# Optimization experiments

Measured on AMD Instinct MI355X. Metric: run time of the kernel, lower is better.

## Reference

```python
import jax, jax.numpy as jnp
import numpy as np

EMBED_DIM = 1024
NUM_HEADS = 16
HEAD_DIM = EMBED_DIM // NUM_HEADS
GLOBAL_HEADS = 1
LOCAL_K = 128
SCALE = HEAD_DIM ** -0.5


def setup_inputs() -> dict:
    key = jax.random.key(0)
    ks = jax.random.split(key, 9)
    B, n = 4, 2048
    s = 1.0 / np.sqrt(EMBED_DIM)  # torch Linear default uniform(-1/sqrt(in), 1/sqrt(in))
    def lin(k):
        kw, kb = jax.random.split(k)
        W = jax.random.uniform(kw, (EMBED_DIM, EMBED_DIM), jnp.float32, -s, s)
        b = jax.random.uniform(kb, (EMBED_DIM,), jnp.float32, -s, s)
        return W, b
    wq, bq = lin(ks[0])
    wk, bk = lin(ks[1])
    wv, bv = lin(ks[2])
    wo, bo = lin(ks[3])
    x = jax.random.normal(ks[4], (B, n, EMBED_DIM), jnp.float32)
    return {"x": x, "wq": wq, "bq": bq, "wk": wk, "bk": bk,
            "wv": wv, "bv": bv, "wo": wo, "bo": bo}


def _attend(x, wq, bq, wk, bk, wv, bv, wo, bo):
    B, n, E = x.shape
    H, D = NUM_HEADS, HEAD_DIM
    def proj(W, b):
        t = x @ W.T + b                       # [B, n, E]
        return t.reshape(B, n, H, D).transpose(0, 2, 1, 3)  # [B, H, n, D]
    q, k, v = proj(wq, bq), proj(wk, bk), proj(wv, bv)
    scores = jnp.einsum('bhqd,bhkd->bhqk', q, k) * SCALE  # [B, H, n, n]
    idx = jnp.arange(n)
    band = jnp.abs(idx[:, None] - idx[None, :]) <= LOCAL_K  # [n, n] True = allowed
    is_global = jnp.arange(H) < GLOBAL_HEADS
    mask = band[None, :, :] | is_global[:, None, None]      # [H, n, n]
    scores = jnp.where(mask[None], scores, -jnp.inf)
    attn = jax.nn.softmax(scores, axis=-1)   # dropout is identity (p=0 / eval)
    out = jnp.einsum('bhqk,bhkd->bhqd', attn, v)
    out = out.transpose(0, 2, 1, 3).reshape(B, n, E)
    return out @ wo.T + bo


def reference(x, wq, bq, wk, bk, wv, bv, wo, bo):
    return _attend(x, wq, bq, wk, bk, wv, bv, wo, bo)
```

## Files before the change

### kernel.cpp

```cpp
#include <hip/hip_runtime.h>

typedef __attribute__((ext_vector_type(4))) float f32x4;
typedef __attribute__((ext_vector_type(8))) short s16x8;

#define GLDS(gsrc, ldst) \
  __builtin_amdgcn_global_load_lds((const __attribute__((address_space(1))) void*)(gsrc), \
                                   (__attribute__((address_space(3))) void*)(ldst), 16, 0, 0)

__device__ __forceinline__ ushort f2bf(float f) {
  union { float f; unsigned u; } x; x.f = f;
  unsigned r = (x.u + 0x7FFFu + ((x.u >> 16) & 1u)) >> 16;
  return (ushort)r;
}

__global__ __launch_bounds__(256) void castk(const float* __restrict__ in,
                                             ushort* __restrict__ outp, int n) {
  int i = (blockIdx.x * 256 + threadIdx.x) * 4;
  if (i >= n) return;
  float4 v = *(const float4*)(in + i);
  ushort4 r;
  r.x = f2bf(v.x); r.y = f2bf(v.y); r.z = f2bf(v.z); r.w = f2bf(v.w);
  *(ushort4*)(outp + i) = r;
}

__global__ __launch_bounds__(256) void castw(const float* __restrict__ w0, const float* __restrict__ w1,
                                             const float* __restrict__ w2, const float* __restrict__ w3,
                                             ushort* __restrict__ o0, ushort* __restrict__ o1,
                                             ushort* __restrict__ o2, ushort* __restrict__ o3) {
  int bid = blockIdx.x;
  int sel = bid >> 10;
  const float* in = (sel == 0) ? w0 : (sel == 1) ? w1 : (sel == 2) ? w2 : w3;
  ushort* outp    = (sel == 0) ? o0 : (sel == 1) ? o1 : (sel == 2) ? o2 : o3;
  int i = ((bid & 1023) * 256 + threadIdx.x) * 4;
  float4 v = *(const float4*)(in + i);
  ushort4 r;
  r.x = f2bf(v.x); r.y = f2bf(v.y); r.z = f2bf(v.z); r.w = f2bf(v.w);
  *(ushort4*)(outp + i) = r;
}

#define BM 128
#define BN 128
#define BK 32

__global__ __launch_bounds__(256) void gemm_bt(
    const ushort* __restrict__ A, const ushort* __restrict__ Bt,
    const float* __restrict__ bias0, const float* __restrict__ bias1,
    const float* __restrict__ bias2,
    void* __restrict__ Cout, int M, int N, int K, int outBf16)
{
  __shared__ __align__(16) ushort As[BM * BK];
  __shared__ __align__(16) ushort Bs[BN * BK];
  const int tid = threadIdx.x;
  const int w = tid >> 6, lane = tid & 63;
  const int wr = w >> 1, wc = w & 1;
  const int lrow = lane & 15, lg = lane >> 4;
  const int mblk = blockIdx.y * BM, nblk = blockIdx.x * BN;
  const int c0 = 2 * w, c1 = 2 * w + 1;
  const int ar0 = 16 * c0 + (lane >> 2), ar1 = 16 * c1 + (lane >> 2);
  const int akk = 8 * (lane & 3);
  const ushort* Ab = A + (size_t)mblk * K + akk;
  const ushort* Bb = Bt + (size_t)nblk * K + akk;
  const f32x4 zero = {0.f, 0.f, 0.f, 0.f};
  f32x4 acc[4][4];
#pragma unroll
  for (int m = 0; m < 4; m++)
#pragma unroll
    for (int n = 0; n < 4; n++) acc[m][n] = zero;

  for (int kt = 0; kt < K; kt += BK) {
    GLDS(Ab + (size_t)ar0 * K + kt, &As[512 * c0]);
    GLDS(Ab + (size_t)ar1 * K + kt, &As[512 * c1]);
    GLDS(Bb + (size_t)ar0 * K + kt, &Bs[512 * c0]);
    GLDS(Bb + (size_t)ar1 * K + kt, &Bs[512 * c1]);
    __syncthreads();
    s16x8 af[4], bfr[4];
#pragma unroll
    for (int m = 0; m < 4; m++)
      af[m] = *(const s16x8*)&As[(64 * wr + 16 * m + lrow) * BK + 8 * lg];
#pragma unroll
    for (int n = 0; n < 4; n++)
      bfr[n] = *(const s16x8*)&Bs[(64 * wc + 16 * n + lrow) * BK + 8 * lg];
#pragma unroll
    for (int m = 0; m < 4; m++)
#pragma unroll
      for (int n = 0; n < 4; n++)
        acc[m][n] = __builtin_amdgcn_mfma_f32_16x16x32_bf16(af[m], bfr[n], acc[m][n], 0, 0, 0);
    __syncthreads();
  }

#pragma unroll
  for (int m = 0; m < 4; m++) {
    const int row = mblk + 64 * wr + 16 * m + 4 * lg;
#pragma unroll
    for (int n = 0; n < 4; n++) {
      const int col = nblk + 64 * wc + 16 * n + lrow;
      float bias;
      if (bias1) bias = (col < 1024) ? bias0[col]
                       : (col < 2048 ? bias1[col - 1024] : bias2[col - 2048]);
      else bias = bias0[col];
      f32x4 v = acc[m][n];
      if (outBf16) {
        ushort* C = (ushort*)Cout;
#pragma unroll
        for (int i = 0; i < 4; i++) C[(size_t)(row + i) * N + col] = f2bf(v[i] + bias);
      } else {
        float* C = (float*)Cout;
#pragma unroll
        for (int i = 0; i < 4; i++) C[(size_t)(row + i) * N + col] = v[i] + bias;
      }
    }
  }
}

__global__ __launch_bounds__(256) void attn_kernel(const ushort* __restrict__ qkv,
                                                   ushort* __restrict__ outp,
                                                   float* __restrict__ oPart,
                                                   float* __restrict__ mPart,
                                                   float* __restrict__ lPart)
{
  __shared__ __align__(16) ushort Ks[64 * 64];
  __shared__ __align__(16) ushort Vt[64 * 64];
  __shared__ __align__(16) ushort Ps[4][16 * 40];

  const int tid = threadIdx.x;
  const int w = tid >> 6, lane = tid & 63;
  const int lrow = lane & 15, lg = lane >> 4;

  const int bid = (blockIdx.x & 7) * 368 + (blockIdx.x >> 3);
  int h, b, bx, kv_lo, kv_hi, chunk = 0;
  bool isGlobal;
  if (bid < 1024) {
    isGlobal = true; h = 0;
    chunk = bid >> 7;
    int qb = bid & 127;
    b = qb >> 5; bx = qb & 31;
    kv_lo = chunk * 256; kv_hi = kv_lo + 256;
  } else {
    isGlobal = false;
    int t = bid - 1024;
    h = 1 + (t >> 7);
    int qb = t & 127;
    b = qb >> 5; bx = qb & 31;
    kv_lo = bx * 64 - 128; if (kv_lo < 0) kv_lo = 0;
    kv_hi = bx * 64 + 192; if (kv_hi > 2048) kv_hi = 2048;
  }
  const int q0b = bx * 64;
  const int q0 = q0b + w * 16;
  const ushort* Qp = qkv + (size_t)b * 2048 * 3072 + h * 64;
  const ushort* Kp = Qp + 1024;
  const ushort* Vp = Qp + 2048;

  s16x8 qf0 = *(const s16x8*)(Qp + (size_t)(q0 + lrow) * 3072 + 8 * lg);
  s16x8 qf1 = *(const s16x8*)(Qp + (size_t)(q0 + lrow) * 3072 + 32 + 8 * lg);

  const f32x4 zero = {0.f, 0.f, 0.f, 0.f};
  f32x4 o[4];
  o[0] = zero; o[1] = zero; o[2] = zero; o[3] = zero;
  float mrun = -3e38f, lsum = 0.f;
  const int q_abs = q0 + lrow;
  const float SCL = 0.18033688011112042f;

  const int sp = tid >> 3;
  const int sg = tid & 7;
  const int kr0 = tid >> 3;
  const int kc = tid & 7;
  const int vx = (lrow & 7) ^ (lrow >> 3);

  for (int kv = kv_lo; kv < kv_hi; kv += 64) {
    const bool needMask = !isGlobal && (kv < q0b - 64 || kv + 64 > q0b + 128);

    const ushort* vrow = Vp + (size_t)(kv + 2 * sp) * 3072 + 8 * sg;
    s16x8 vlo = *(const s16x8*)vrow;
    s16x8 vhi = *(const s16x8*)(vrow + 3072);

    __syncthreads();

    GLDS(Kp + (size_t)(kv + kr0) * 3072 + 8 * (kc ^ (kr0 & 7)), &Ks[w * 512]);
    GLDS(Kp + (size_t)(kv + 32 + kr0) * 3072 + 8 * (kc ^ (kr0 & 7)), &Ks[2048 + w * 512]);

#pragma unroll
    for (int j = 0; j < 8; j++) {
      const int d = 8 * sg + j;
      const int r = 2 * sp;
      uint pk = (uint)(ushort)vlo[j] | ((uint)(ushort)vhi[j] << 16);
      *(uint*)&Vt[d * 64 + ((((r >> 3) ^ j ^ sg) & 7) << 3) + (r & 7)] = pk;
    }
    __syncthreads();

#pragma unroll
    for (int s = 0; s < 2; s++) {
      const int kb = kv + 32 * s;
      const int rs = 32 * s;
      s16x8 kA0 = *(const s16x8*)&Ks[(rs + lrow) * 64      + ((( lg      ^ (lrow & 7)) & 7) << 3)];
      s16x8 kA1 = *(const s16x8*)&Ks[(rs + lrow) * 64      + ((((4 + lg) ^ (lrow & 7)) & 7) << 3)];
      s16x8 kB0 = *(const s16x8*)&Ks[(rs + 16 + lrow) * 64 + ((( lg      ^ (lrow & 7)) & 7) << 3)];
      s16x8 kB1 = *(const s16x8*)&Ks[(rs + 16 + lrow) * 64 + ((((4 + lg) ^ (lrow & 7)) & 7) << 3)];

      f32x4 sA = __builtin_amdgcn_mfma_f32_16x16x32_bf16(kA0, qf0, zero, 0, 0, 0);
      sA = __builtin_amdgcn_mfma_f32_16x16x32_bf16(kA1, qf1, sA, 0, 0, 0);
      f32x4 sB = __builtin_amdgcn_mfma_f32_16x16x32_bf16(kB0, qf0, zero, 0, 0, 0);
      sB = __builtin_amdgcn_mfma_f32_16x16x32_bf16(kB1, qf1, sB, 0, 0, 0);

      float pA[4], pB[4];
      float rowmax = -3e38f;
      if (needMask) {
#pragma unroll
        for (int i = 0; i < 4; i++) {
          int kaA = kb + 4 * lg + i;
          int dq = q_abs - kaA;
          float va = (dq <= 128 && dq >= -128) ? sA[i] * SCL : -1e30f;
          pA[i] = va; rowmax = fmaxf(rowmax, va);
          int dqb = dq - 16;
          float vb = (dqb <= 128 && dqb >= -128) ? sB[i] * SCL : -1e30f;
          pB[i] = vb; rowmax = fmaxf(rowmax, vb);
        }
      } else {
#pragma unroll
        for (int i = 0; i < 4; i++) {
          pA[i] = sA[i] * SCL; pB[i] = sB[i] * SCL;
          rowmax = fmaxf(rowmax, fmaxf(pA[i], pB[i]));
        }
      }
      rowmax = fmaxf(rowmax, __shfl_xor(rowmax, 16));
      rowmax = fmaxf(rowmax, __shfl_xor(rowmax, 32));

      if (!__all(rowmax <= mrun + 8.f)) {
        float mnew = fmaxf(mrun, rowmax);
        float alpha = exp2f(mrun - mnew);
        mrun = mnew;
        lsum *= alpha;
        float a0 = __shfl(alpha, 4 * lg + 0);
        float a1 = __shfl(alpha, 4 * lg + 1);
        float a2 = __shfl(alpha, 4 * lg + 2);
        float a3 = __shfl(alpha, 4 * lg + 3);
#pragma unroll
        for (int c = 0; c < 4; c++) {
          o[c][0] *= a0; o[c][1] *= a1; o[c][2] *= a2; o[c][3] *= a3;
        }
      }

      float rsum = 0.f;
      if (needMask) {
#pragma unroll
        for (int i = 0; i < 4; i++) {
          pA[i] = (pA[i] > -1e29f) ? exp2f(pA[i] - mrun) : 0.f;
          pB[i] = (pB[i] > -1e29f) ? exp2f(pB[i] - mrun) : 0.f;
          rsum += pA[i] + pB[i];
        }
      } else {
#pragma unroll
        for (int i = 0; i < 4; i++) {
          pA[i] = exp2f(pA[i] - mrun);
          pB[i] = exp2f(pB[i] - mrun);
          rsum += pA[i] + pB[i];
        }
      }
      rsum += __shfl_xor(rsum, 16);
      rsum += __shfl_xor(rsum, 32);
      lsum += rsum;

      {
        ushort* P = &Ps[w][lrow * 40];
        *(uint*)&P[4 * lg]      = (uint)f2bf(pA[0]) | ((uint)f2bf(pA[1]) << 16);
        *(uint*)&P[4 * lg + 2]  = (uint)f2bf(pA[2]) | ((uint)f2bf(pA[3]) << 16);
        *(uint*)&P[16 + 4 * lg] = (uint)f2bf(pB[0]) | ((uint)f2bf(pB[1]) << 16);
        *(uint*)&P[18 + 4 * lg] = (uint)f2bf(pB[2]) | ((uint)f2bf(pB[3]) << 16);
      }
      s16x8 paf = *(const s16x8*)&Ps[w][lrow * 40 + 8 * lg];

#pragma unroll
      for (int c = 0; c < 4; c++) {
        const int d = 16 * c + lrow;
        s16x8 vf = *(const s16x8*)&Vt[d * 64 + ((((4 * s + lg) ^ vx ^ (2 * c)) & 7) << 3)];
        o[c] = __builtin_amdgcn_mfma_f32_16x16x32_bf16(paf, vf, o[c], 0, 0, 0);
      }
    }
  }

  if (isGlobal) {
    const size_t rbase = (size_t)(chunk * 4 + b) * 2048 + q0;
    if (lg == 0) {
      mPart[rbase + lrow] = mrun;
      lPart[rbase + lrow] = lsum;
    }
#pragma unroll
    for (int c = 0; c < 4; c++)
#pragma unroll
      for (int i = 0; i < 4; i++)
        oPart[(rbase + 4 * lg + i) * 64 + 16 * c + lrow] = o[c][i];
  } else {
    float li0 = 1.f / __shfl(lsum, 4 * lg + 0);
    float li1 = 1.f / __shfl(lsum, 4 * lg + 1);
    float li2 = 1.f / __shfl(lsum, 4 * lg + 2);
    float li3 = 1.f / __shfl(lsum, 4 * lg + 3);
    size_t orow = (size_t)(b * 2048 + q0 + 4 * lg);
#pragma unroll
    for (int c = 0; c < 4; c++) {
      outp[(orow + 0) * 1024 + h * 64 + 16 * c + lrow] = f2bf(o[c][0] * li0);
      outp[(orow + 1) * 1024 + h * 64 + 16 * c + lrow] = f2bf(o[c][1] * li1);
      outp[(orow + 2) * 1024 + h * 64 + 16 * c + lrow] = f2bf(o[c][2] * li2);
      outp[(orow + 3) * 1024 + h * 64 + 16 * c + lrow] = f2bf(o[c][3] * li3);
    }
  }
}

__global__ __launch_bounds__(256) void combine_kernel(const float* __restrict__ oPart,
                                                      const float* __restrict__ mPart,
                                                      const float* __restrict__ lPart,
                                                      ushort* __restrict__ attno) {
  const int tid = threadIdx.x;
  const int row = blockIdx.x * 64 + (tid >> 2);
  const int d0 = (tid & 3) * 16;
  float m[8], l[8], M = -3e38f;
#pragma unroll
  for (int p = 0; p < 8; p++) {
    m[p] = mPart[p * 8192 + row];
    l[p] = lPart[p * 8192 + row];
    M = fmaxf(M, m[p]);
  }
  float L = 0.f, wgt[8];
#pragma unroll
  for (int p = 0; p < 8; p++) { wgt[p] = exp2f(m[p] - M); L += wgt[p] * l[p]; }
  float inv = 1.f / L;
  float acc[16];
#pragma unroll
  for (int j = 0; j < 16; j++) acc[j] = 0.f;
#pragma unroll
  for (int p = 0; p < 8; p++) {
    const float* op = oPart + ((size_t)p * 8192 + row) * 64 + d0;
    float wv = wgt[p];
#pragma unroll
    for (int j = 0; j < 16; j += 4) {
      float4 v = *(const float4*)(op + j);
      acc[j]     += wv * v.x; acc[j + 1] += wv * v.y;
      acc[j + 2] += wv * v.z; acc[j + 3] += wv * v.w;
    }
  }
  ushort* dst = attno + (size_t)row * 1024 + d0;
#pragma unroll
  for (int j = 0; j < 16; j++) dst[j] = f2bf(acc[j] * inv);
}

extern "C" void kernel_launch(void* const* d_in, const int* in_sizes, int n_in,
                              void* d_out, int out_size, void* d_ws, size_t ws_size,
                              hipStream_t stream) {
  const float* x  = (const float*)d_in[0];
  const float* wq = (const float*)d_in[1];
  const float* bq = (const float*)d_in[2];
  const float* wk = (const float*)d_in[3];
  const float* bk = (const float*)d_in[4];
  const float* wv = (const float*)d_in[5];
  const float* bv = (const float*)d_in[6];
  const float* wo = (const float*)d_in[7];
  const float* bo = (const float*)d_in[8];

  char* ws = (char*)d_ws;
  ushort* xb    = (ushort*)(ws);
  ushort* wqkvb = (ushort*)(ws + 16777216);
  ushort* wob   = (ushort*)(ws + 23068672);
  ushort* qkvb  = (ushort*)(ws + 25165824);
  ushort* attno = (ushort*)(ws + 75497472);
  float* oPart = (float*)(ws);
  float* mPart = (float*)(ws + 16777216);
  float* lPart = (float*)(ws + 16777216 + 262144);

  castk<<<8192, 256, 0, stream>>>(x, xb, 8388608);
  castw<<<4096, 256, 0, stream>>>(wq, wk, wv, wo,
                                  wqkvb, wqkvb + 1048576, wqkvb + 2097152, wob);

  gemm_bt<<<dim3(24, 64), 256, 0, stream>>>(xb, wqkvb, bq, bk, bv,
                                            (void*)qkvb, 8192, 3072, 1024, 1);

  attn_kernel<<<2944, 256, 0, stream>>>(qkvb, attno, oPart, mPart, lPart);
  combine_kernel<<<128, 256, 0, stream>>>(oPart, mPart, lPart, attno);

  gemm_bt<<<dim3(8, 64), 256, 0, stream>>>(attno, wob, bo, nullptr, nullptr,
                                           (void*)d_out, 8192, 1024, 1024, 0);
}
```

Baseline: 183.4 us.

## Replace GEMM with 128x256 triple-buffered swizzled-LDS kernel and coalesced epilogue

Replaces the simple 128x128 single-buffer GEMM with a 512-thread 128x256-tile kernel. It uses BK=64, a three-stage global_load_lds pipeline with explicit vmcnt waits, and an XOR-swizzled LDS layout to avoid bank conflicts. It also adds a remapping of workgroup IDs across XCDs and s_setprio around the MFMA bursts. The epilogue now stages results through LDS so global stores are wide and coalesced instead of scattered scalar writes. The cost is higher LDS use (144KB), which limits occupancy, plus more complex wait-count logic.

```diff
diff --git a/kernel.cpp b/kernel.cpp
--- a/kernel.cpp
+++ b/kernel.cpp
@@ -38,28 +38,50 @@
   *(ushort4*)(outp + i) = r;
 }
 
-#define BM 128
-#define BN 128
-#define BK 32
-
-__global__ __launch_bounds__(256) void gemm_bt(
+template<int OUTBF16>
+__global__ __launch_bounds__(512, 2) void gemm256(
     const ushort* __restrict__ A, const ushort* __restrict__ Bt,
     const float* __restrict__ bias0, const float* __restrict__ bias1,
     const float* __restrict__ bias2,
-    void* __restrict__ Cout, int M, int N, int K, int outBf16)
+    void* __restrict__ Cout, int M, int N, int K, int nxn)
 {
-  __shared__ __align__(16) ushort As[BM * BK];
-  __shared__ __align__(16) ushort Bs[BN * BK];
+  __shared__ __align__(16) ushort lds[73728];
   const int tid = threadIdx.x;
   const int w = tid >> 6, lane = tid & 63;
-  const int wr = w >> 1, wc = w & 1;
   const int lrow = lane & 15, lg = lane >> 4;
-  const int mblk = blockIdx.y * BM, nblk = blockIdx.x * BN;
-  const int c0 = 2 * w, c1 = 2 * w + 1;
-  const int ar0 = 16 * c0 + (lane >> 2), ar1 = 16 * c1 + (lane >> 2);
-  const int akk = 8 * (lane & 3);
-  const ushort* Ab = A + (size_t)mblk * K + akk;
-  const ushort* Bb = Bt + (size_t)nblk * K + akk;
+  const int wm = w >> 2, wn = w & 3;
+  const int cpx = gridDim.x >> 3;
+  const int wgid = ((int)blockIdx.x & 7) * cpx + ((int)blockIdx.x >> 3);
+  const int mblk = (wgid / nxn) * 128;
+  const int nblk = (wgid % nxn) * 256;
+  const int NT = K >> 6;
+
+  const int srow = tid >> 3;
+  const int scol = 8 * ((tid & 7) ^ (srow & 7));
+  const ushort* Abase = A + (size_t)(mblk + srow) * K + scol;
+  const ushort* Bbase = Bt + (size_t)(nblk + srow) * K + scol;
+  const size_t rstep = (size_t)64 * K;
+  const int dA = w * 512;
+  const int dB = 8192 + w * 512;
+
+#define STAGE_A(kt, bf) { \
+    GLDS(Abase + (size_t)(kt) * 64,         &lds[(bf) * 24576 + dA]); \
+    GLDS(Abase + (size_t)(kt) * 64 + rstep, &lds[(bf) * 24576 + dA + 4096]); }
+#define STAGE_B(kt, bf) { \
+    GLDS(Bbase + (size_t)(kt) * 64,             &lds[(bf) * 24576 + dB]); \
+    GLDS(Bbase + (size_t)(kt) * 64 + rstep,     &lds[(bf) * 24576 + dB + 4096]); \
+    GLDS(Bbase + (size_t)(kt) * 64 + 2 * rstep, &lds[(bf) * 24576 + dB + 8192]); \
+    GLDS(Bbase + (size_t)(kt) * 64 + 3 * rstep, &lds[(bf) * 24576 + dB + 12288]); }
+
+  int offA[4][2], offB[4][2];
+#pragma unroll
+  for (int m = 0; m < 4; m++)
+#pragma unroll
+    for (int kk = 0; kk < 2; kk++) {
+      offA[m][kk] = (wm * 64 + m * 16 + lrow) * 64 + (((kk * 4 + lg) ^ (lrow & 7)) << 3);
+      offB[m][kk] = 8192 + (wn * 64 + m * 16 + lrow) * 64 + (((kk * 4 + lg) ^ (lrow & 7)) << 3);
+    }
+
   const f32x4 zero = {0.f, 0.f, 0.f, 0.f};
   f32x4 acc[4][4];
 #pragma unroll
@@ -67,47 +89,99 @@
 #pragma unroll
     for (int n = 0; n < 4; n++) acc[m][n] = zero;
 
-  for (int kt = 0; kt < K; kt += BK) {
-    GLDS(Ab + (size_t)ar0 * K + kt, &As[512 * c0]);
-    GLDS(Ab + (size_t)ar1 * K + kt, &As[512 * c1]);
-    GLDS(Bb + (size_t)ar0 * K + kt, &Bs[512 * c0]);
-    GLDS(Bb + (size_t)ar1 * K + kt, &Bs[512 * c1]);
+  STAGE_A(0, 0); STAGE_B(0, 0);
+  if (NT > 1) { STAGE_A(1, 1); STAGE_B(1, 1); }
+
+  int b = 0;
+  for (int t = 0; t < NT; ++t) {
+    if (t < NT - 1) { asm volatile("s_waitcnt vmcnt(6)" ::: "memory"); }
+    else            { asm volatile("s_waitcnt vmcnt(0)" ::: "memory"); }
+    __builtin_amdgcn_s_barrier();
+    const int bb = b * 24576;
+    const int t2 = t + 2;
+    const int b2 = (b >= 1) ? b - 1 : 2;
+
+    if (t2 < NT) STAGE_A(t2, b2);
+    {
+      s16x8 af[4], bf_[4];
+#pragma unroll
+      for (int m = 0; m < 4; m++) af[m] = *(const s16x8*)&lds[bb + offA[m][0]];
+#pragma unroll
+      for (int n = 0; n < 4; n++) bf_[n] = *(const s16x8*)&lds[bb + offB[n][0]];
+      __builtin_amdgcn_s_setprio(1);
+#pragma unroll
+      for (int m = 0; m < 4; m++)
+#pragma unroll
+        for (int n = 0; n < 4; n++)
+          acc[m][n] = __builtin_amdgcn_mfma_f32_16x16x32_bf16(af[m], bf_[n], acc[m][n], 0, 0, 0);
+      __builtin_amdgcn_s_setprio(0);
+    }
+    if (t2 < NT) STAGE_B(t2, b2);
+    {
+      s16x8 af[4], bf_[4];
+#pragma unroll
+      for (int m = 0; m < 4; m++) af[m] = *(const s16x8*)&lds[bb + offA[m][1]];
+#pragma unroll
+      for (int n = 0; n < 4; n++) bf_[n] = *(const s16x8*)&lds[bb + offB[n][1]];
+      __builtin_amdgcn_s_setprio(1);
+#pragma unroll
+      for (int m = 0; m < 4; m++)
+#pragma unroll
+        for (int n = 0; n < 4; n++)
+          acc[m][n] = __builtin_amdgcn_mfma_f32_16x16x32_bf16(af[m], bf_[n], acc[m][n], 0, 0, 0);
+      __builtin_amdgcn_s_setprio(0);
+    }
+    b = (b == 2) ? 0 : b + 1;
+  }
+#undef STAGE_A
+#undef STAGE_B
+
+  float bias_n[4];
+#pragma unroll
+  for (int n = 0; n < 4; n++) {
+    const int col = nblk + wn * 64 + n * 16 + lrow;
+    if (bias1) bias_n[n] = (col < 1024) ? bias0[col]
+                          : (col < 2048 ? bias1[col - 1024] : bias2[col - 2048]);
+    else bias_n[n] = bias0[col];
+  }
+
+  __syncthreads();
+
+  if (OUTBF16) {
+    ushort* Ct = lds;
+#pragma unroll
+    for (int m = 0; m < 4; m++)
+#pragma unroll
+      for (int n = 0; n < 4; n++)
+#pragma unroll
+        for (int i = 0; i < 4; i++)
+          Ct[(wm * 64 + m * 16 + 4 * lg + i) * 256 + wn * 64 + n * 16 + lrow] =
+              f2bf(acc[m][n][i] + bias_n[n]);
     __syncthreads();
-    s16x8 af[4], bfr[4];
+    ushort* Cg = (ushort*)Cout;
+#pragma unroll
+    for (int r = 0; r < 8; r++) {
+      const int row = r * 16 + (tid >> 5);
+      const int col = (tid & 31) * 8;
+      *(s16x8*)&Cg[(size_t)(mblk + row) * N + nblk + col] = *(const s16x8*)&lds[r * 4096 + tid * 8];
+    }
+  } else {
+    float* Cf = (float*)lds;
 #pragma unroll
     for (int m = 0; m < 4; m++)
-      af[m] = *(const s16x8*)&As[(64 * wr + 16 * m + lrow) * BK + 8 * lg];
-#pragma unroll
-    for (int n = 0; n < 4; n++)
-      bfr[n] = *(const s16x8*)&Bs[(64 * wc + 16 * n + lrow) * BK + 8 * lg];
-#pragma unroll
-    for (int m = 0; m < 4; m++)
 #pragma unroll
       for (int n = 0; n < 4; n++)
-        acc[m][n] = __builtin_amdgcn_mfma_f32_16x16x32_bf16(af[m], bfr[n], acc[m][n], 0, 0, 0);
+#pragma unroll
+        for (int i = 0; i < 4; i++)
+          Cf[(wm * 64 + m * 16 + 4 * lg + i) * 256 + wn * 64 + n * 16 + lrow] =
+              acc[m][n][i] + bias_n[n];
     __syncthreads();
-  }
-
-#pragma unroll
-  for (int m = 0; m < 4; m++) {
-    const int row = mblk + 64 * wr + 16 * m + 4 * lg;
-#pragma unroll
-    for (int n = 0; n < 4; n++) {
-      const int col = nblk + 64 * wc + 16 * n + lrow;
-      float bias;
-      if (bias1) bias = (col < 1024) ? bias0[col]
-                       : (col < 2048 ? bias1[col - 1024] : bias2[col - 2048]);
-      else bias = bias0[col];
-      f32x4 v = acc[m][n];
-      if (outBf16) {
-        ushort* C = (ushort*)Cout;
-#pragma unroll
-        for (int i = 0; i < 4; i++) C[(size_t)(row + i) * N + col] = f2bf(v[i] + bias);
-      } else {
-        float* C = (float*)Cout;
-#pragma unroll
-        for (int i = 0; i < 4; i++) C[(size_t)(row + i) * N + col] = v[i] + bias;
-      }
+    float* Cg = (float*)Cout;
+#pragma unroll
+    for (int r = 0; r < 16; r++) {
+      const int row = r * 8 + (tid >> 6);
+      const int col = (tid & 63) * 4;
+      *(float4*)&Cg[(size_t)(mblk + row) * N + nblk + col] = *(const float4*)&Cf[r * 2048 + tid * 4];
     }
   }
 }
@@ -368,12 +442,12 @@
   castw<<<4096, 256, 0, stream>>>(wq, wk, wv, wo,
                                   wqkvb, wqkvb + 1048576, wqkvb + 2097152, wob);
 
-  gemm_bt<<<dim3(24, 64), 256, 0, stream>>>(xb, wqkvb, bq, bk, bv,
-                                            (void*)qkvb, 8192, 3072, 1024, 1);
+  gemm256<1><<<768, 512, 0, stream>>>(xb, wqkvb, bq, bk, bv,
+                                      (void*)qkvb, 8192, 3072, 1024, 12);
 
   attn_kernel<<<2944, 256, 0, stream>>>(qkvb, attno, oPart, mPart, lPart);
   combine_kernel<<<128, 256, 0, stream>>>(oPart, mPart, lPart, attno);
 
-  gemm_bt<<<dim3(8, 64), 256, 0, stream>>>(attno, wob, bo, nullptr, nullptr,
-                                           (void*)d_out, 8192, 1024, 1024, 0);
-}
+  gemm256<0><<<256, 512, 0, stream>>>(attno, wob, bo, nullptr, nullptr,
+                                      (void*)d_out, 8192, 1024, 1024, 4);
+}
```

Result: faster. 167.1 us (-8.9%).

## Replace GEMM with 256x256 tile, double-buffered, swizzled LDS pipelined kernel

Applied to the files above, without the earlier changes.

Replaces the simple 128x128x32 single-buffer bf16 GEMM with a 512-thread 256x256 tile kernel using BK=64, double-buffered LDS fed by global_load_lds, XOR-swizzled LDS layout, and a quadrant-interleaved schedule that overlaps loads with MFMA. It adds explicit vmcnt waits, setprio around MFMA bursts, XCD-aware block remapping, and an LDS-staged epilogue that writes output in coalesced vectors. The goal is to remove stalls from the synchronous load/compute loop and uncoalesced stores. The larger tiles yield fewer workgroups (384 and 128), which may underfill the GPU, especially for the output projection.

```diff
diff --git a/kernel.cpp b/kernel.cpp
--- a/kernel.cpp
+++ b/kernel.cpp
@@ -11,6 +11,12 @@
   union { float f; unsigned u; } x; x.f = f;
   unsigned r = (x.u + 0x7FFFu + ((x.u >> 16) & 1u)) >> 16;
   return (ushort)r;
+}
+
+template<int N> __device__ __forceinline__ void waitvm() {
+  if constexpr (N == 0) asm volatile("s_waitcnt vmcnt(0)" ::: "memory");
+  else if constexpr (N == 4) asm volatile("s_waitcnt vmcnt(4)" ::: "memory");
+  else if constexpr (N == 8) asm volatile("s_waitcnt vmcnt(8)" ::: "memory");
 }
 
 __global__ __launch_bounds__(256) void castk(const float* __restrict__ in,
@@ -38,75 +44,184 @@
   *(ushort4*)(outp + i) = r;
 }
 
-#define BM 128
-#define BN 128
-#define BK 32
-
-__global__ __launch_bounds__(256) void gemm_bt(
+template<int OUTBF16>
+__global__ __launch_bounds__(512) void gemmQ(
     const ushort* __restrict__ A, const ushort* __restrict__ Bt,
     const float* __restrict__ bias0, const float* __restrict__ bias1,
     const float* __restrict__ bias2,
-    void* __restrict__ Cout, int M, int N, int K, int outBf16)
+    void* __restrict__ Cout, int M, int N, int K, int nxn)
 {
-  __shared__ __align__(16) ushort As[BM * BK];
-  __shared__ __align__(16) ushort Bs[BN * BK];
+  constexpr int SB = 32768;
+  __shared__ __align__(16) ushort lds[65536];
+
   const int tid = threadIdx.x;
   const int w = tid >> 6, lane = tid & 63;
-  const int wr = w >> 1, wc = w & 1;
   const int lrow = lane & 15, lg = lane >> 4;
-  const int mblk = blockIdx.y * BM, nblk = blockIdx.x * BN;
-  const int c0 = 2 * w, c1 = 2 * w + 1;
-  const int ar0 = 16 * c0 + (lane >> 2), ar1 = 16 * c1 + (lane >> 2);
-  const int akk = 8 * (lane & 3);
-  const ushort* Ab = A + (size_t)mblk * K + akk;
-  const ushort* Bb = Bt + (size_t)nblk * K + akk;
+  const int wm2a = (w >> 2) * 64, wn2a = (w & 3) * 32;
+  const int cpx = gridDim.x >> 3;
+  const int wgid = ((int)blockIdx.x & 7) * cpx + ((int)blockIdx.x >> 3);
+  const int mblk = (wgid / nxn) * 256;
+  const int nblk = (wgid % nxn) * 256;
+  const int NT = K >> 6, NI = NT >> 1;
+
+  const int sg8 = 8 * ((tid & 7) ^ ((tid >> 3) & 7));
+  const ushort* As0 = A + (size_t)(mblk + (tid >> 3)) * K + sg8;
+  const ushort* Bs0 = Bt + (size_t)(nblk + (tid >> 3)) * K + sg8;
+  const size_t r64 = (size_t)64 * K;
+  const int wl512 = w * 512;
+
+  auto stage = [&](int isB, int kt, int half, int bufb) {
+    const ushort* s = (isB ? Bs0 : As0) + (size_t)kt * 64 + (size_t)(half * 128) * K;
+    const int d = bufb + isB * 16384 + half * 8192 + wl512;
+    GLDS(s, &lds[d]);
+    GLDS(s + r64, &lds[d + 4096]);
+  };
+
+  const int axk0 = ((lg) ^ (lrow & 7)) << 3;
+  const int axk1 = ((4 + lg) ^ (lrow & 7)) << 3;
+  const int arow = (wm2a + lrow) * 64;
+  const int brow = 16384 + (wn2a + lrow) * 64;
+
+  s16x8 af[4][2], bf0[2][2], bf1[2][2];
   const f32x4 zero = {0.f, 0.f, 0.f, 0.f};
-  f32x4 acc[4][4];
-#pragma unroll
-  for (int m = 0; m < 4; m++)
-#pragma unroll
-    for (int n = 0; n < 4; n++) acc[m][n] = zero;
-
-  for (int kt = 0; kt < K; kt += BK) {
-    GLDS(Ab + (size_t)ar0 * K + kt, &As[512 * c0]);
-    GLDS(Ab + (size_t)ar1 * K + kt, &As[512 * c1]);
-    GLDS(Bb + (size_t)ar0 * K + kt, &Bs[512 * c0]);
-    GLDS(Bb + (size_t)ar1 * K + kt, &Bs[512 * c1]);
+  f32x4 acc[2][2][4][2];
+#pragma unroll
+  for (int qm = 0; qm < 2; qm++)
+#pragma unroll
+    for (int qn = 0; qn < 2; qn++)
+#pragma unroll
+      for (int mf = 0; mf < 4; mf++)
+#pragma unroll
+        for (int nf = 0; nf < 2; nf++) acc[qm][qn][mf][nf] = zero;
+
+#define LOADA(qm, bb) { \
+  _Pragma("unroll") for (int mf = 0; mf < 4; mf++) { \
+    af[mf][0] = *(const s16x8*)&lds[(bb) + (qm) * 8192 + arow + mf * 1024 + axk0]; \
+    af[mf][1] = *(const s16x8*)&lds[(bb) + (qm) * 8192 + arow + mf * 1024 + axk1]; } }
+#define LOADB(qn, bb, bfr) { \
+  _Pragma("unroll") for (int nf = 0; nf < 2; nf++) { \
+    bfr[nf][0] = *(const s16x8*)&lds[(bb) + (qn) * 8192 + brow + nf * 1024 + axk0]; \
+    bfr[nf][1] = *(const s16x8*)&lds[(bb) + (qn) * 8192 + brow + nf * 1024 + axk1]; } }
+#define MMA(qm, qn, bfr) { \
+  __builtin_amdgcn_s_setprio(1); \
+  _Pragma("unroll") for (int mf = 0; mf < 4; mf++) \
+    _Pragma("unroll") for (int nf = 0; nf < 2; nf++) { \
+      acc[qm][qn][mf][nf] = __builtin_amdgcn_mfma_f32_16x16x32_bf16(af[mf][0], bfr[nf][0], acc[qm][qn][mf][nf], 0, 0, 0); \
+      acc[qm][qn][mf][nf] = __builtin_amdgcn_mfma_f32_16x16x32_bf16(af[mf][1], bfr[nf][1], acc[qm][qn][mf][nf], 0, 0, 0); } \
+  __builtin_amdgcn_s_setprio(0); }
+#define BAR() __builtin_amdgcn_s_barrier()
+
+  stage(0, 0, 0, 0);  stage(0, 0, 1, 0);  stage(1, 0, 0, 0);  stage(1, 0, 1, 0);
+  stage(0, 1, 0, SB); stage(0, 1, 1, SB); stage(1, 1, 0, SB); stage(1, 1, 1, SB);
+  waitvm<8>(); BAR();
+
+  for (int it = 0; it < NI; ++it) {
+    const bool sB1 = (it > 0);
+    const bool sA2 = (2 * it + 2 < NT);
+    const bool sB2 = (2 * it + 3 < NT);
+    const int kb1 = 2 * it + 1, ka2 = 2 * it + 2, kb2 = 2 * it + 3;
+
+    LOADA(0, 0); LOADB(0, 0, bf0);
+    if (sB1) stage(0, kb1, 1, SB);
+    BAR(); MMA(0, 0, bf0); BAR();
+    LOADB(1, 0, bf1);
+    if (sB1) stage(1, kb1, 0, SB);
+    BAR(); MMA(0, 1, bf1); BAR();
+    LOADA(1, 0);
+    if (sA2) stage(0, ka2, 0, 0);
+    BAR(); MMA(1, 1, bf1);
+    BAR();
+    if (sA2) stage(1, ka2, 1, 0);
+    BAR(); MMA(1, 0, bf0);
+    if (it == NI - 1) waitvm<0>(); else waitvm<4>();
+    BAR();
+
+    LOADA(0, SB); LOADB(0, SB, bf0);
+    if (sA2) stage(0, ka2, 1, 0);
+    BAR(); MMA(0, 0, bf0); BAR();
+    LOADB(1, SB, bf1);
+    if (sA2) stage(1, ka2, 0, 0);
+    BAR(); MMA(0, 1, bf1); BAR();
+    LOADA(1, SB);
+    if (sB2) stage(0, kb2, 0, SB);
+    BAR(); MMA(1, 1, bf1); BAR();
+    if (sB2) stage(1, kb2, 1, SB);
+    BAR(); MMA(1, 0, bf0);
+    if (it + 1 < NI) {
+      if (it + 1 == NI - 1) waitvm<0>(); else waitvm<4>();
+      BAR();
+    }
+  }
+#undef LOADA
+#undef LOADB
+#undef MMA
+#undef BAR
+
+  float bias_n[2][2];
+#pragma unroll
+  for (int qn = 0; qn < 2; qn++)
+#pragma unroll
+    for (int nf = 0; nf < 2; nf++) {
+      const int col = nblk + qn * 128 + wn2a + nf * 16 + lrow;
+      if (bias1) bias_n[qn][nf] = (col < 1024) ? bias0[col]
+                                 : (col < 2048 ? bias1[col - 1024] : bias2[col - 2048]);
+      else bias_n[qn][nf] = bias0[col];
+    }
+
+  __syncthreads();
+
+  if constexpr (OUTBF16) {
+    ushort* Ct = lds;
+#pragma unroll
+    for (int qm = 0; qm < 2; qm++)
+#pragma unroll
+      for (int qn = 0; qn < 2; qn++)
+#pragma unroll
+        for (int mf = 0; mf < 4; mf++)
+#pragma unroll
+          for (int nf = 0; nf < 2; nf++) {
+            f32x4 v = acc[qm][qn][mf][nf];
+#pragma unroll
+            for (int i = 0; i < 4; i++)
+              Ct[(qm * 128 + wm2a + mf * 16 + 4 * lg + i) * 256 +
+                 qn * 128 + wn2a + nf * 16 + lrow] = f2bf(v[i] + bias_n[qn][nf]);
+          }
     __syncthreads();
-    s16x8 af[4], bfr[4];
-#pragma unroll
-    for (int m = 0; m < 4; m++)
-      af[m] = *(const s16x8*)&As[(64 * wr + 16 * m + lrow) * BK + 8 * lg];
-#pragma unroll
-    for (int n = 0; n < 4; n++)
-      bfr[n] = *(const s16x8*)&Bs[(64 * wc + 16 * n + lrow) * BK + 8 * lg];
-#pragma unroll
-    for (int m = 0; m < 4; m++)
-#pragma unroll
-      for (int n = 0; n < 4; n++)
-        acc[m][n] = __builtin_amdgcn_mfma_f32_16x16x32_bf16(af[m], bfr[n], acc[m][n], 0, 0, 0);
-    __syncthreads();
-  }
-
-#pragma unroll
-  for (int m = 0; m < 4; m++) {
-    const int row = mblk + 64 * wr + 16 * m + 4 * lg;
-#pragma unroll
-    for (int n = 0; n < 4; n++) {
-      const int col = nblk + 64 * wc + 16 * n + lrow;
-      float bias;
-      if (bias1) bias = (col < 1024) ? bias0[col]
-                       : (col < 2048 ? bias1[col - 1024] : bias2[col - 2048]);
-      else bias = bias0[col];
-      f32x4 v = acc[m][n];
-      if (outBf16) {
-        ushort* C = (ushort*)Cout;
-#pragma unroll
-        for (int i = 0; i < 4; i++) C[(size_t)(row + i) * N + col] = f2bf(v[i] + bias);
-      } else {
-        float* C = (float*)Cout;
-#pragma unroll
-        for (int i = 0; i < 4; i++) C[(size_t)(row + i) * N + col] = v[i] + bias;
+    ushort* Cg = (ushort*)Cout;
+#pragma unroll
+    for (int p = 0; p < 16; p++) {
+      const unsigned g = p * 512 + tid;
+      const unsigned row = g >> 5, c8 = g & 31;
+      *(s16x8*)&Cg[(size_t)(mblk + row) * N + nblk + c8 * 8] = *(const s16x8*)&lds[g * 8];
+    }
+  } else {
+    float* Cf = (float*)lds;
+    float* Cg = (float*)Cout;
+#pragma unroll
+    for (int c = 0; c < 4; c++) {
+      __syncthreads();
+      if ((w >> 2) == (c & 1)) {
+        const int qm = c >> 1;
+#pragma unroll
+        for (int qn = 0; qn < 2; qn++)
+#pragma unroll
+          for (int mf = 0; mf < 4; mf++)
+#pragma unroll
+            for (int nf = 0; nf < 2; nf++) {
+              f32x4 v = acc[qm][qn][mf][nf];
+#pragma unroll
+              for (int i = 0; i < 4; i++)
+                Cf[(mf * 16 + 4 * lg + i) * 256 + qn * 128 + wn2a + nf * 16 + lrow] =
+                    v[i] + bias_n[qn][nf];
+            }
+      }
+      __syncthreads();
+#pragma unroll
+      for (int p = 0; p < 8; p++) {
+        const unsigned fg = p * 512 + tid;
+        const unsigned row = fg >> 6, c4 = fg & 63;
+        *(float4*)&Cg[(size_t)(mblk + c * 64 + row) * N + nblk + c4 * 4] =
+            *(const float4*)&Cf[fg * 4];
       }
     }
   }
@@ -368,12 +483,12 @@
   castw<<<4096, 256, 0, stream>>>(wq, wk, wv, wo,
                                   wqkvb, wqkvb + 1048576, wqkvb + 2097152, wob);
 
-  gemm_bt<<<dim3(24, 64), 256, 0, stream>>>(xb, wqkvb, bq, bk, bv,
-                                            (void*)qkvb, 8192, 3072, 1024, 1);
+  gemmQ<1><<<384, 512, 0, stream>>>(xb, wqkvb, bq, bk, bv,
+                                    (void*)qkvb, 8192, 3072, 1024, 12);
 
   attn_kernel<<<2944, 256, 0, stream>>>(qkvb, attno, oPart, mPart, lPart);
   combine_kernel<<<128, 256, 0, stream>>>(oPart, mPart, lPart, attno);
 
-  gemm_bt<<<dim3(8, 64), 256, 0, stream>>>(attno, wob, bo, nullptr, nullptr,
-                                           (void*)d_out, 8192, 1024, 1024, 0);
-}
+  gemmQ<0><<<128, 512, 0, stream>>>(attno, wob, bo, nullptr, nullptr,
+                                    (void*)d_out, 8192, 1024, 1024, 4);
+}
```

New measurement: 174.1 us. 5.1% less time.
